# Performance work log

Hardware: AMD Instinct MI355X
Metric: run time of the kernel (lower is better)

## Reference

```python
import jax, jax.numpy as jnp
import numpy as np

B = 8192
FEATURE_NUM = 200      # categorical fields
NUMERIC_SIZE = 100     # dense features
FEATURE_SIZE = 1_000_000  # vocab for one-hot weights
EMBED = 64
OUT_DIM = 1


def setup_inputs() -> dict:
    key = jax.random.key(0)
    k_idx, k_num, k_w1, k_w2, k_v1, k_v2 = jax.random.split(key, 6)
    # first FEATURE_NUM columns are categorical indices stored as floats
    idx = jax.random.randint(k_idx, (B, FEATURE_NUM), 0, FEATURE_SIZE).astype(jnp.float32)
    numeric = jax.random.normal(k_num, (B, NUMERIC_SIZE), dtype=jnp.float32)
    inputs = jnp.concatenate([idx, numeric], axis=1)  # [B, 300]
    scale = 0.05
    return {
        "inputs": inputs,
        "w_one_hot": jax.random.normal(k_w1, (FEATURE_SIZE, OUT_DIM), dtype=jnp.float32) * scale,
        "w_numeric": jax.random.normal(k_w2, (NUMERIC_SIZE, OUT_DIM), dtype=jnp.float32) * scale,
        "v_one_hot": jax.random.normal(k_v1, (FEATURE_SIZE, EMBED), dtype=jnp.float32) * scale,
        "v_numeric": jax.random.normal(k_v2, (NUMERIC_SIZE, EMBED), dtype=jnp.float32) * scale,
        "b": jnp.zeros((OUT_DIM,), dtype=jnp.float32),
    }


def reference(inputs, w_one_hot, w_numeric, v_one_hot, v_numeric, b):
    # split categorical indices / numeric features
    idx = inputs[:, :FEATURE_NUM].astype(jnp.int32)   # [B, F]
    numeric = inputs[:, FEATURE_NUM:]                 # [B, N]

    # first order: gathered scalar weights (output_dim==1) + linear on numeric
    first_order = jnp.sum(w_one_hot[idx, 0], axis=1) + jnp.sum(numeric @ w_numeric, axis=1)  # [B]

    # second order FM: 0.5 * sum_e ((sum_f v)^2 - sum_f v^2) over concatenated fields
    sec_w = v_one_hot[idx]                            # [B, F, E] gathered embeddings
    num_w = numeric[:, :, None] * v_numeric[None]     # [B, N, E]
    field_sum = jnp.sum(sec_w, axis=1) + jnp.sum(num_w, axis=1)            # [B, E]
    field_sq_sum = jnp.sum(sec_w * sec_w, axis=1) + jnp.sum(num_w * num_w, axis=1)  # [B, E]
    second_order = 0.5 * jnp.sum(field_sum * field_sum - field_sq_sum, axis=1)      # [B]

    out = first_order + second_order + b[0]
    return out[:, None]  # [B, 1]
```

## Files before the change

### kernel.cpp

```cpp
#include <hip/hip_runtime.h>

#define BATCH 8192
#define FEATURE_NUM 200
#define NUMERIC_SIZE 100
#define IN_STRIDE (FEATURE_NUM + NUMERIC_SIZE)
#define EMBED 64
#define WAVES_PER_BLOCK 4

__global__ __launch_bounds__(256, 8) void fm_layer_kernel(
    const float* __restrict__ inputs,
    const float* __restrict__ w_one_hot,
    const float* __restrict__ w_numeric,
    const float* __restrict__ v_one_hot,
    const float* __restrict__ v_numeric,
    const float* __restrict__ bias,
    float* __restrict__ out)
{
    __shared__ int   s_idx[WAVES_PER_BLOCK][FEATURE_NUM];
    __shared__ float s_num[WAVES_PER_BLOCK][NUMERIC_SIZE];

    const int lane = threadIdx.x & 63;
    const int wave = threadIdx.x >> 6;
    const int row  = blockIdx.x * WAVES_PER_BLOCK + wave;

    const float* in_row = inputs + (size_t)row * IN_STRIDE;

    for (int j = lane; j < IN_STRIDE; j += 64) {
        float x = in_row[j];
        if (j < FEATURE_NUM) s_idx[wave][j] = (int)x;
        else                 s_num[wave][j - FEATURE_NUM] = x;
    }
    __syncthreads();

    float fs = 0.f, fss = 0.f, first = 0.f;

    #pragma unroll 1
    for (int c = 0; c < 192; c += 16) {
        int   idx[16];
        float v[16];
        #pragma unroll
        for (int s = 0; s < 16; ++s) idx[s] = s_idx[wave][c + s];
        #pragma unroll
        for (int s = 0; s < 16; ++s) v[s] = v_one_hot[(size_t)idx[s] * EMBED + lane];
        #pragma unroll
        for (int s = 0; s < 16; ++s) { fs += v[s]; fss += v[s] * v[s]; }
    }
    {
        int idx[8]; float v[8];
        #pragma unroll
        for (int s = 0; s < 8; ++s) idx[s] = s_idx[wave][192 + s];
        #pragma unroll
        for (int s = 0; s < 8; ++s) v[s] = v_one_hot[(size_t)idx[s] * EMBED + lane];
        #pragma unroll
        for (int s = 0; s < 8; ++s) { fs += v[s]; fss += v[s] * v[s]; }
    }

    #pragma unroll 1
    for (int j = 0; j < NUMERIC_SIZE; j += 10) {
        #pragma unroll
        for (int s = 0; s < 10; ++s) {
            float x  = s_num[wave][j + s];
            float v  = v_numeric[(j + s) * EMBED + lane];
            float nv = x * v;
            fs += nv; fss += nv * nv;
        }
    }

    #pragma unroll
    for (int k = 0; k < 4; ++k) {
        int j = lane + 64 * k;
        if (j < FEATURE_NUM) first += w_one_hot[s_idx[wave][j]];
    }
    #pragma unroll
    for (int k = 0; k < 2; ++k) {
        int j = lane + 64 * k;
        if (j < NUMERIC_SIZE) first += s_num[wave][j] * w_numeric[j];
    }

    float partial = first + 0.5f * (fs * fs - fss);

    #pragma unroll
    for (int off = 32; off > 0; off >>= 1)
        partial += __shfl_down(partial, off, 64);

    if (lane == 0) out[row] = partial + bias[0];
}

extern "C" void kernel_launch(void* const* d_in, const int* in_sizes, int n_in,
                              void* d_out, int out_size, void* d_ws, size_t ws_size,
                              hipStream_t stream) {
    const float* inputs    = (const float*)d_in[0];
    const float* w_one_hot = (const float*)d_in[1];
    const float* w_numeric = (const float*)d_in[2];
    const float* v_one_hot = (const float*)d_in[3];
    const float* v_numeric = (const float*)d_in[4];
    const float* bias      = (const float*)d_in[5];
    float* out = (float*)d_out;

    dim3 grid(BATCH / WAVES_PER_BLOCK);
    dim3 block(256);
    fm_layer_kernel<<<grid, block, 0, stream>>>(
        inputs, w_one_hot, w_numeric, v_one_hot, v_numeric, bias, out);
}
```

Baseline: 374.9 us.

## Gather embeddings with float4 loads across four sub-groups and double-buffer

Each wave is split into four 16-lane groups that each fetch a full 256-byte embedding row as float4, so one wave instruction gathers four rows instead of one. Loads are software-pipelined with two register buffers to keep gathers in flight while accumulating the previous batch. Partial sums are combined across sub-groups with xor shuffles before the FM term is formed. The changes raise per-thread register use and add a cross-group reduction step.

```diff
diff --git a/kernel.cpp b/kernel.cpp
--- a/kernel.cpp
+++ b/kernel.cpp
@@ -6,6 +6,28 @@
 #define IN_STRIDE (FEATURE_NUM + NUMERIC_SIZE)
 #define EMBED 64
 #define WAVES_PER_BLOCK 4
+
+
+__device__ __forceinline__ void load4(const float4* __restrict__ vtab,
+                                      const int* sidx, int base, int sub,
+                                      int l, float4 vv[4]) {
+    #pragma unroll
+    for (int i = 0; i < 4; ++i) {
+        int idx = sidx[base + i * 4 + sub];
+        vv[i] = vtab[(size_t)idx * 16 + l];
+    }
+}
+
+__device__ __forceinline__ void acc4(const float4 vv[4],
+                                     float4& fs, float4& fss) {
+    #pragma unroll
+    for (int i = 0; i < 4; ++i) {
+        fs.x += vv[i].x; fss.x += vv[i].x * vv[i].x;
+        fs.y += vv[i].y; fss.y += vv[i].y * vv[i].y;
+        fs.z += vv[i].z; fss.z += vv[i].z * vv[i].z;
+        fs.w += vv[i].w; fss.w += vv[i].w * vv[i].w;
+    }
+}
 
 __global__ __launch_bounds__(256, 8) void fm_layer_kernel(
     const float* __restrict__ inputs,
@@ -21,6 +43,8 @@
 
     const int lane = threadIdx.x & 63;
     const int wave = threadIdx.x >> 6;
+    const int sub  = lane >> 4;
+    const int l    = lane & 15;
     const int row  = blockIdx.x * WAVES_PER_BLOCK + wave;
 
     const float* in_row = inputs + (size_t)row * IN_STRIDE;
@@ -32,52 +56,72 @@
     }
     __syncthreads();
 
-    float fs = 0.f, fss = 0.f, first = 0.f;
+    const int*   sidx = s_idx[wave];
+    const float* snum = s_num[wave];
+    const float4* vtab = (const float4*)v_one_hot;
+    const float4* ntab = (const float4*)v_numeric;
+
+    float4 fs4  = {0.f, 0.f, 0.f, 0.f};
+    float4 fss4 = {0.f, 0.f, 0.f, 0.f};
+
+    float4 va[4], vb[4];
+    load4(vtab, sidx, 0, sub, l, va);
 
     #pragma unroll 1
-    for (int c = 0; c < 192; c += 16) {
-        int   idx[16];
-        float v[16];
+    for (int jj = 0; jj < 25; jj += 5) {
         #pragma unroll
-        for (int s = 0; s < 16; ++s) idx[s] = s_idx[wave][c + s];
-        #pragma unroll
-        for (int s = 0; s < 16; ++s) v[s] = v_one_hot[(size_t)idx[s] * EMBED + lane];
-        #pragma unroll
-        for (int s = 0; s < 16; ++s) { fs += v[s]; fss += v[s] * v[s]; }
-    }
-    {
-        int idx[8]; float v[8];
-        #pragma unroll
-        for (int s = 0; s < 8; ++s) idx[s] = s_idx[wave][192 + s];
-        #pragma unroll
-        for (int s = 0; s < 8; ++s) v[s] = v_one_hot[(size_t)idx[s] * EMBED + lane];
-        #pragma unroll
-        for (int s = 0; s < 8; ++s) { fs += v[s]; fss += v[s] * v[s]; }
+        for (int t = 0; t < 5; ++t) {
+            int j = (jj + t) * 4 + sub;
+            float  x = snum[j];
+            float4 v = ntab[(size_t)j * 16 + l];
+            float nx = x * v.x, ny = x * v.y, nz = x * v.z, nw = x * v.w;
+            fs4.x += nx; fss4.x += nx * nx;
+            fs4.y += ny; fss4.y += ny * ny;
+            fs4.z += nz; fss4.z += nz * nz;
+            fs4.w += nw; fss4.w += nw * nw;
+        }
     }
 
     #pragma unroll 1
-    for (int j = 0; j < NUMERIC_SIZE; j += 10) {
-        #pragma unroll
-        for (int s = 0; s < 10; ++s) {
-            float x  = s_num[wave][j + s];
-            float v  = v_numeric[(j + s) * EMBED + lane];
-            float nv = x * v;
-            fs += nv; fss += nv * nv;
-        }
+    for (int k = 0; k < 5; ++k) {
+        load4(vtab, sidx, (2 * k + 1) * 16, sub, l, vb);
+        acc4(va, fs4, fss4);
+        load4(vtab, sidx, (2 * k + 2) * 16, sub, l, va);
+        acc4(vb, fs4, fss4);
+    }
+    load4(vtab, sidx, 11 * 16, sub, l, vb);
+    acc4(va, fs4, fss4);
+    float4 t0, t1;
+    { int i0 = sidx[192 + sub]; t0 = vtab[(size_t)i0 * 16 + l];
+      int i1 = sidx[196 + sub]; t1 = vtab[(size_t)i1 * 16 + l]; }
+    acc4(vb, fs4, fss4);
+    fs4.x += t0.x + t1.x; fss4.x += t0.x * t0.x + t1.x * t1.x;
+    fs4.y += t0.y + t1.y; fss4.y += t0.y * t0.y + t1.y * t1.y;
+    fs4.z += t0.z + t1.z; fss4.z += t0.z * t0.z + t1.z * t1.z;
+    fs4.w += t0.w + t1.w; fss4.w += t0.w * t0.w + t1.w * t1.w;
+
+    #pragma unroll
+    for (int off = 16; off <= 32; off <<= 1) {
+        fs4.x  += __shfl_xor(fs4.x,  off, 64);
+        fs4.y  += __shfl_xor(fs4.y,  off, 64);
+        fs4.z  += __shfl_xor(fs4.z,  off, 64);
+        fs4.w  += __shfl_xor(fs4.w,  off, 64);
+        fss4.x += __shfl_xor(fss4.x, off, 64);
+        fss4.y += __shfl_xor(fss4.y, off, 64);
+        fss4.z += __shfl_xor(fss4.z, off, 64);
+        fss4.w += __shfl_xor(fss4.w, off, 64);
     }
 
-    #pragma unroll
-    for (int k = 0; k < 4; ++k) {
-        int j = lane + 64 * k;
-        if (j < FEATURE_NUM) first += w_one_hot[s_idx[wave][j]];
-    }
-    #pragma unroll
-    for (int k = 0; k < 2; ++k) {
-        int j = lane + 64 * k;
-        if (j < NUMERIC_SIZE) first += s_num[wave][j] * w_numeric[j];
-    }
+    float so4 = 0.5f * ((fs4.x * fs4.x - fss4.x) + (fs4.y * fs4.y - fss4.y) +
+                        (fs4.z * fs4.z - fss4.z) + (fs4.w * fs4.w - fss4.w));
+    float partial = (sub == 0) ? so4 : 0.f;
 
-    float partial = first + 0.5f * (fs * fs - fss);
+    partial += w_one_hot[sidx[lane]];
+    partial += w_one_hot[sidx[lane + 64]];
+    partial += w_one_hot[sidx[lane + 128]];
+    if (lane < 8) partial += w_one_hot[sidx[192 + lane]];
+    partial += snum[lane] * w_numeric[lane];
+    if (lane < NUMERIC_SIZE - 64) partial += snum[lane + 64] * w_numeric[lane + 64];
 
     #pragma unroll
     for (int off = 32; off > 0; off >>= 1)
```

New measurement: 375.7 us. Within noise of the previous version (+0.2%).
